# Kernel optimization log

Hardware: AMD Instinct MI355X
Metric: run time of the kernel (lower is better)

## Reference

```python
import jax, jax.numpy as jnp
import numpy as np

TAU = 0.5

def setup_inputs() -> dict:
    key = jax.random.key(0)
    ks = jax.random.split(key, 20)
    B, D1, D2, E1, E2, U = 4096, 2000, 2000, 256, 256, 512
    M = E1 + E2
    s = lambda k, shp, scale=0.05: jax.random.normal(k, shp, dtype=jnp.float32) * scale
    return {
        "inputs": jax.random.normal(ks[0], (B, D1 + D2), dtype=jnp.float32),
        "h_tm1": jax.random.normal(ks[1], (B, U), dtype=jnp.float32),
        "crohis_tm": jax.random.normal(ks[2], (B, M), dtype=jnp.float32),
        "embed_weight_1": s(ks[3], (D1, E1)),
        "embed_weight_2": s(ks[4], (D2, E2)),
        "ca_1to2_w": s(ks[5], (E1, E1)),
        "ca_1to2_u": s(ks[6], (E2, E1)),
        "ca_1to2_v": s(ks[7], (E2, E1)),
        "ca_2to1_w": s(ks[8], (E2, E2)),
        "ca_2to1_u": s(ks[9], (E1, E2)),
        "ca_2to1_v": s(ks[10], (E1, E2)),
        "crohis_weight_w": s(ks[11], (M, U)),
        "crohis_bias": jnp.zeros((U,), jnp.float32),
        "crohis_decomp_weight": s(ks[12], (M, M)),
        "crohis_decomp_bias": jnp.zeros((M,), jnp.float32),
        "kernel": s(ks[13], (M, 3 * U)),
        "recurrent_kernel": s(ks[14], (U, 3 * U)),
        "bias": jnp.zeros((3 * U,), jnp.float32),
    }


def reference(inputs, h_tm1, crohis_tm,
              embed_weight_1, embed_weight_2,
              ca_1to2_w, ca_1to2_u, ca_1to2_v,
              ca_2to1_w, ca_2to1_u, ca_2to1_v,
              crohis_weight_w, crohis_bias,
              crohis_decomp_weight, crohis_decomp_bias,
              kernel, recurrent_kernel, bias):
    D1 = embed_weight_1.shape[0]
    U = recurrent_kernel.shape[0]
    # dual embedding lookups (dense multi-hot x embedding matrix)
    seqx1 = inputs[:, :D1]
    seqx2 = inputs[:, D1:]
    emb1 = seqx1 @ embed_weight_1   # [B, E1]
    emb2 = seqx2 @ embed_weight_2   # [B, E2]
    # cross-attention gates (softmax over feature axis, as K.softmax default)
    att12 = jax.nn.softmax(jnp.tanh(emb1 @ ca_1to2_w + emb2 @ ca_1to2_u) * (emb2 @ ca_1to2_v), axis=-1)
    att21 = jax.nn.softmax(jnp.tanh(emb2 @ ca_2to1_w + emb1 @ ca_2to1_u) * (emb1 @ ca_2to1_v), axis=-1)
    x = jnp.concatenate([emb1 * att12, emb2 * att21], axis=-1)  # [B, M]
    # cross-history decomposition modulating previous hidden state
    cro = jnp.tanh(crohis_tm @ crohis_decomp_weight + crohis_decomp_bias)
    h_prev = h_tm1 + jnp.tanh(cro @ crohis_weight_w + crohis_bias)
    # GRU (implementation=2, reset_after=False)
    mx = x @ kernel + bias                         # [B, 3U]
    x_z, x_r, x_h = mx[:, :U], mx[:, U:2 * U], mx[:, 2 * U:]
    mi = h_prev @ recurrent_kernel[:, :2 * U]      # [B, 2U]
    z = jax.nn.sigmoid(x_z + mi[:, :U])
    r = jax.nn.sigmoid(x_r + mi[:, U:])
    hh = jnp.tanh(x_h + (r * h_prev) @ recurrent_kernel[:, 2 * U:])
    h = z * h_prev + (1.0 - z) * hh
    # updated cross-history state (exponential moving average with tau)
    crohis_new = TAU * crohis_tm + (1.0 - TAU) * x
    return h, crohis_new
```

## Files before the change

kernel.cpp:

```cpp
#include <hip/hip_runtime.h>
#include <hip/hip_bf16.h>
#include <math.h>


#define TAU_F 0.5f

typedef __bf16 bf16x8 __attribute__((ext_vector_type(8)));
typedef __bf16 bf16x4 __attribute__((ext_vector_type(4)));
typedef float f32x4 __attribute__((ext_vector_type(4)));

__device__ __forceinline__ void gload16(const void* g, void* l) {
    __builtin_amdgcn_global_load_lds(
        (const __attribute__((address_space(1))) void*)g,
        (__attribute__((address_space(3))) void*)l, 16, 0, 0);
}

struct SubGemm64 {
    const float* A;
    int lda;
    int Kvalid;
    const __bf16* BT;
    int ldbt;
    float* C;
    int ldc;
    long long strideC;
    int Ksub;
    int nbx;
    int pairSplit;
    int pairAOff;
};

__global__ __launch_bounds__(256) void gemm64_dual(SubGemm64 g1, SubGemm64 g2, int blocks1)
{
    __shared__ __attribute__((aligned(16))) char lds[24576];
    auto As32 = (float (*)[64][32])lds;
    auto Bs   = (__bf16 (*)[64][32])(lds + 16384);

    const int tid = threadIdx.x, w = tid >> 6, l = tid & 63;

    const int gx = gridDim.x;
    const int nwg = gx * (int)gridDim.y;
    const int hw = (int)blockIdx.y * gx + (int)blockIdx.x;
    const int lg = (hw & 7) * (nwg >> 3) + (hw >> 3);
    const int bxl_lin = lg % gx;
    const int by = lg / gx;

    const bool second = bxl_lin >= blocks1;
    const SubGemm64& g = second ? g2 : g1;
    const int bxl = second ? bxl_lin - blocks1 : bxl_lin;
    const int ct = bxl % g.nbx, spl = bxl / g.nbx;
    const int brow = by * 64, bcol = ct * 64;
    const int k_begin = spl * g.Ksub;
    const int nt = g.Ksub >> 5;
    const int aoff = (ct >= g.pairSplit) ? g.pairAOff : 0;

    const float* Ar0 = g.A + aoff + (size_t)(brow + w * 16 + (l >> 3)) * g.lda;
    const float* Ar8 = Ar0 + (size_t)8 * g.lda;
    const int colLane = (l & 7) * 4;
    const int kcl4 = g.Kvalid - 4;
    const __bf16* Bg = g.BT + (size_t)(bcol + w * 16 + (l >> 2)) * g.ldbt
                     + (l & 3) * 8 + k_begin;

    f32x4 acc[2][2] = {};
    const int fr = l & 15, fk = (l >> 4) * 8;
    const int wr = (w >> 1) * 32, wc = (w & 1) * 32;
    const int kmax = (nt - 1) * 32;

#define ISS64(slot)                                                          \
    {                                                                        \
        const int _s = (slot);                                               \
        const int _k = (_s * 32 < kmax) ? _s * 32 : kmax;                    \
        const int _b = _s & 1;                                               \
        int c0 = k_begin + _k + colLane;                                     \
        c0 = c0 < kcl4 ? c0 : kcl4;                                          \
        gload16(Ar0 + c0, &As32[_b][w * 16][0]);                             \
        gload16(Ar8 + c0, &As32[_b][w * 16 + 8][0]);                         \
        gload16(Bg + _k,  &Bs[_b][w * 16][0]);                               \
    }

    ISS64(0) ISS64(1)

    for (int t = 0; t < nt; ++t) {
        asm volatile("s_waitcnt vmcnt(3)" ::: "memory");
        asm volatile("s_waitcnt lgkmcnt(0)" ::: "memory");
        asm volatile("s_barrier" ::: "memory");

        const int bi = t & 1;
        bf16x8 a[2], b[2];
#pragma unroll
        for (int m = 0; m < 2; ++m) {
            f32x4 lo = *(const f32x4*)&As32[bi][wr + m * 16 + fr][fk];
            f32x4 hi = *(const f32x4*)&As32[bi][wr + m * 16 + fr][fk + 4];
#pragma unroll
            for (int z = 0; z < 4; ++z) { a[m][z] = (__bf16)lo[z]; a[m][4 + z] = (__bf16)hi[z]; }
        }
#pragma unroll
        for (int n = 0; n < 2; ++n) b[n] = *(const bf16x8*)&Bs[bi][wc + n * 16 + fr][fk];

#pragma unroll
        for (int m = 0; m < 2; ++m)
#pragma unroll
            for (int n = 0; n < 2; ++n)
                acc[m][n] = __builtin_amdgcn_mfma_f32_16x16x32_bf16(a[m], b[n], acc[m][n], 0, 0, 0);

        asm volatile("s_barrier" ::: "memory");
        ISS64(t + 2)
    }
#undef ISS64

    float* C = g.C + (size_t)spl * g.strideC;
    const int fq = (l >> 4) * 4;
#pragma unroll
    for (int m = 0; m < 2; ++m)
#pragma unroll
        for (int n = 0; n < 2; ++n)
#pragma unroll
            for (int r = 0; r < 4; ++r) {
                int row = brow + wr + m * 16 + fq + r;
                int col = bcol + wc + n * 16 + fr;
                C[(size_t)row * g.ldc + col] = acc[m][n][r];
            }
}

struct SubGemm {
    const void* A;
    int lda;
    int Kvalid;
    const __bf16* BT;
    int ldbt;
    float* C;
    int ldc;
    long long strideC;
    int Ksub;
    int nbx;
    int pairSplit;
    int pairAOff;
    int obf16;
};

__global__ __launch_bounds__(256) void gemm_dual(SubGemm g1, SubGemm g2, int blocks1)
{
    __shared__ __attribute__((aligned(16))) char lds[49152];

    const int tid = threadIdx.x, w = tid >> 6, l = tid & 63;

    const int gx = gridDim.x;
    const int nwg = gx * (int)gridDim.y;
    const int hw = (int)blockIdx.y * gx + (int)blockIdx.x;
    const int lg = (hw & 7) * (nwg >> 3) + (hw >> 3);
    const int bxl_lin = lg % gx;
    const int by = lg / gx;

    const bool second = bxl_lin >= blocks1;
    const SubGemm& g = second ? g2 : g1;
    const int bxl = second ? bxl_lin - blocks1 : bxl_lin;
    const int ct = bxl % g.nbx, spl = bxl / g.nbx;
    const int brow = by * 64, bcol = ct * 128;
    const int k_begin = spl * g.Ksub;
    const int nt = g.Ksub >> 5;
    const int aoff = (ct >= g.pairSplit) ? g.pairAOff : 0;

    const int sbr = w * 32 + (l >> 2);
    const int seg = (l & 3) * 8;

    const __bf16* Bg0 = g.BT + (size_t)(bcol + sbr) * g.ldbt + seg + k_begin;
    const __bf16* Bg1 = Bg0 + (size_t)16 * g.ldbt;

    f32x4 acc[2][4] = {};
    const int fr = l & 15, fk = (l >> 4) * 8;
    const int wr = (w >> 1) * 32, wc = (w & 1) * 64;
    const int kmax = (nt - 1) * 32;

    auto As = (__bf16 (*)[64][32])lds;
    auto Bs = (__bf16 (*)[128][32])(lds + 16384);

    const int sar = w * 16 + (l >> 2);
    const __bf16* Ar = (const __bf16*)g.A + aoff
                     + (size_t)(brow + sar) * g.lda + seg + k_begin;

#define ISSUE_AB(slot)                                                        \
    {                                                                         \
        const int _s = (slot);                                                \
        const int _k = (_s * 32 < kmax) ? _s * 32 : kmax;                     \
        const int _b = _s & 3;                                                \
        gload16(Ar + _k,  &As[_b][w * 16][0]);                                \
        gload16(Bg0 + _k, &Bs[_b][w * 32][0]);                                \
        gload16(Bg1 + _k, &Bs[_b][w * 32 + 16][0]);                           \
    }

    ISSUE_AB(0) ISSUE_AB(1) ISSUE_AB(2)

    for (int t = 0; t < nt; ++t) {
        asm volatile("s_waitcnt vmcnt(6)" ::: "memory");
        asm volatile("s_waitcnt lgkmcnt(0)" ::: "memory");
        __builtin_amdgcn_s_barrier();

        const int bi = t & 3;
        bf16x8 a[2], b[4];
#pragma unroll
        for (int m = 0; m < 2; ++m) a[m] = *(const bf16x8*)&As[bi][wr + m * 16 + fr][fk];
#pragma unroll
        for (int n = 0; n < 4; ++n) b[n] = *(const bf16x8*)&Bs[bi][wc + n * 16 + fr][fk];

        ISSUE_AB(t + 3)

#pragma unroll
        for (int m = 0; m < 2; ++m)
#pragma unroll
            for (int n = 0; n < 4; ++n)
                acc[m][n] = __builtin_amdgcn_mfma_f32_16x16x32_bf16(a[m], b[n], acc[m][n], 0, 0, 0);
    }
#undef ISSUE_AB

    const int fq = (l >> 4) * 4;
    if (g.obf16) {
        __bf16* Cb = (__bf16*)g.C + (size_t)spl * g.strideC;
#pragma unroll
        for (int m = 0; m < 2; ++m)
#pragma unroll
            for (int n = 0; n < 4; ++n)
#pragma unroll
                for (int r = 0; r < 4; ++r) {
                    int row = brow + wr + m * 16 + fq + r;
                    int col = bcol + wc + n * 16 + fr;
                    Cb[(size_t)row * g.ldc + col] = (__bf16)acc[m][n][r];
                }
    } else {
        float* C = g.C + (size_t)spl * g.strideC;
#pragma unroll
        for (int m = 0; m < 2; ++m)
#pragma unroll
            for (int n = 0; n < 4; ++n)
#pragma unroll
                for (int r = 0; r < 4; ++r) {
                    int row = brow + wr + m * 16 + fq + r;
                    int col = bcol + wc + n * 16 + fr;
                    C[(size_t)row * g.ldc + col] = acc[m][n][r];
                }
    }
}

__global__ __launch_bounds__(256) void gemm_g8(
    const __bf16* __restrict__ A, const __bf16* __restrict__ BT,
    const float* __restrict__ mx, const float* __restrict__ mi2,
    const float* __restrict__ hprev, const float* __restrict__ bias,
    float* __restrict__ h)
{
    __shared__ __attribute__((aligned(16))) char lds[49152];

    const int tid = threadIdx.x, w = tid >> 6, l = tid & 63;

    const int gx = gridDim.x;
    const int nwg = gx * (int)gridDim.y;
    const int hw = (int)blockIdx.y * gx + (int)blockIdx.x;
    const int lg = (hw & 7) * (nwg >> 3) + (hw >> 3);
    const int ct = lg % gx;
    const int by = lg / gx;

    const int brow = by * 64, bcol = ct * 128;
    const int nt = 16;

    const int sbr = w * 32 + (l >> 2);
    const int seg = (l & 3) * 8;

    const __bf16* Bg0 = BT + (size_t)(bcol + sbr) * 512 + seg;
    const __bf16* Bg1 = Bg0 + (size_t)16 * 512;

    f32x4 acc[2][4] = {};
    const int fr = l & 15, fk = (l >> 4) * 8;
    const int wr = (w >> 1) * 32, wc = (w & 1) * 64;
    const int kmax = (nt - 1) * 32;

    auto As = (__bf16 (*)[64][32])lds;
    auto Bs = (__bf16 (*)[128][32])(lds + 16384);

    const int sar = w * 16 + (l >> 2);
    const __bf16* Ar = A + (size_t)(brow + sar) * 512 + seg;

#define ISSUE_G8(slot)                                                        \
    {                                                                         \
        const int _s = (slot);                                                \
        const int _k = (_s * 32 < kmax) ? _s * 32 : kmax;                     \
        const int _b = _s & 3;                                                \
        gload16(Ar + _k,  &As[_b][w * 16][0]);                                \
        gload16(Bg0 + _k, &Bs[_b][w * 32][0]);                                \
        gload16(Bg1 + _k, &Bs[_b][w * 32 + 16][0]);                           \
    }

    ISSUE_G8(0) ISSUE_G8(1) ISSUE_G8(2)

    for (int t = 0; t < nt; ++t) {
        asm volatile("s_waitcnt vmcnt(6)" ::: "memory");
        asm volatile("s_waitcnt lgkmcnt(0)" ::: "memory");
        __builtin_amdgcn_s_barrier();

        const int bi = t & 3;
        bf16x8 a[2], b[4];
#pragma unroll
        for (int m = 0; m < 2; ++m) a[m] = *(const bf16x8*)&As[bi][wr + m * 16 + fr][fk];
#pragma unroll
        for (int n = 0; n < 4; ++n) b[n] = *(const bf16x8*)&Bs[bi][wc + n * 16 + fr][fk];

        ISSUE_G8(t + 3)

#pragma unroll
        for (int m = 0; m < 2; ++m)
#pragma unroll
            for (int n = 0; n < 4; ++n)
                acc[m][n] = __builtin_amdgcn_mfma_f32_16x16x32_bf16(a[m], b[n], acc[m][n], 0, 0, 0);
    }
#undef ISSUE_G8

    const int fq = (l >> 4) * 4;
#pragma unroll
    for (int m = 0; m < 2; ++m)
#pragma unroll
        for (int n = 0; n < 4; ++n)
#pragma unroll
            for (int r = 0; r < 4; ++r) {
                int row = brow + wr + m * 16 + fq + r;
                int col = bcol + wc + n * 16 + fr;
                float xz = mx[(size_t)row * 1536 + col]        + bias[col];
                float xh = mx[(size_t)row * 1536 + 1024 + col] + bias[1024 + col];
                float mz = mi2[(size_t)row * 1024 + col];
                float hp = hprev[(size_t)row * 512 + col];
                float z  = 1.f / (1.f + expf(-(xz + mz)));
                float hh = tanhf(xh + acc[m][n][r]);
                h[(size_t)row * 512 + col] = z * hp + (1.f - z) * hh;
            }
}

__global__ __launch_bounds__(256) void prep_wT(
    const float* __restrict__ ew1, const float* __restrict__ ew2,
    const float* __restrict__ w12, const float* __restrict__ u12,
    const float* __restrict__ v12, const float* __restrict__ w21,
    const float* __restrict__ u21, const float* __restrict__ v21,
    const float* __restrict__ cd_w, const float* __restrict__ cw_w,
    const float* __restrict__ kern, const float* __restrict__ rkern,
    __bf16* __restrict__ WT, __bf16* __restrict__ WcatT,
    __bf16* __restrict__ cdT, __bf16* __restrict__ cwT,
    __bf16* __restrict__ kernT, __bf16* __restrict__ rkernT)
{
    __shared__ float tile[64][65];
    const int b = blockIdx.x, tid = threadIdx.x;
    const int tr = tid >> 6, tc = tid & 63;

    const float* src = nullptr;
    int ldsrc = 0, srow0 = 0, scol0 = 0, kvalid = 1 << 30;
    __bf16* dst; int ldd, n0, k0;
    bool zero = false;

    if (b < 256) {
        int q = b; n0 = (q >> 5) * 64; k0 = (q & 31) * 64;
        dst = WT; ldd = 2048; kvalid = 2000; ldsrc = 256; srow0 = k0;
        if (n0 < 256) { src = ew1; scol0 = n0; } else { src = ew2; scol0 = n0 - 256; }
    } else if (b < 384) {
        int q = b - 256; n0 = (q >> 3) * 64; k0 = (q & 7) * 64;
        dst = WcatT; ldd = 512; ldsrc = 256; srow0 = k0 & 255; scol0 = n0 & 255;
        int qn = n0 >> 8; bool khi = k0 >= 256;
        if (qn == 0)      src = khi ? u12 : w12;
        else if (qn == 1) src = khi ? w21 : u21;
        else if (qn == 2) { if (khi) src = v12; else zero = true; }
        else              { if (khi) zero = true; else src = v21; }
    } else if (b < 448) {
        int q = b - 384; n0 = (q >> 3) * 64; k0 = (q & 7) * 64;
        src = cd_w; ldsrc = 512; srow0 = k0; scol0 = n0; dst = cdT; ldd = 512;
    } else if (b < 512) {
        int q = b - 448; n0 = (q >> 3) * 64; k0 = (q & 7) * 64;
        src = cw_w; ldsrc = 512; srow0 = k0; scol0 = n0; dst = cwT; ldd = 512;
    } else if (b < 704) {
        int q = b - 512; n0 = (q >> 3) * 64; k0 = (q & 7) * 64;
        src = kern; ldsrc = 1536; srow0 = k0; scol0 = n0; dst = kernT; ldd = 512;
    } else {
        int q = b - 704; n0 = (q >> 3) * 64; k0 = (q & 7) * 64;
        src = rkern; ldsrc = 1536; srow0 = k0; scol0 = n0; dst = rkernT; ldd = 512;
    }

#pragma unroll
    for (int p = 0; p < 16; ++p) {
        int kr = p * 4 + tr;
        float v = 0.f;
        if (!zero && (srow0 + kr) < kvalid)
            v = src[(size_t)(srow0 + kr) * ldsrc + scol0 + tc];
        tile[kr][tc] = v;
    }
    __syncthreads();
#pragma unroll
    for (int p = 0; p < 16; ++p) {
        int nr = p * 4 + tr;
        dst[(size_t)(n0 + nr) * ldd + k0 + tc] = (__bf16)tile[tc][nr];
    }
}

__global__ __launch_bounds__(256) void reduce_A(
    const float* __restrict__ P12, const float* __restrict__ P4,
    const float* __restrict__ cd_b,
    __bf16* __restrict__ E, __bf16* __restrict__ cro)
{
    const int S = 1 << 21;
    int b = blockIdx.x;
    int i = (((b & 2047) * 256) + threadIdx.x) * 4;
    if (b < 2048) {
        f32x4 p0 = *(const f32x4*)(P12 + i);
        f32x4 p1 = *(const f32x4*)(P12 + S + i);
        f32x4 p2 = *(const f32x4*)(P12 + 2 * S + i);
        f32x4 p3 = *(const f32x4*)(P12 + 3 * S + i);
        __bf16 o[4];
#pragma unroll
        for (int j = 0; j < 4; ++j) o[j] = (__bf16)((p0[j] + p1[j]) + (p2[j] + p3[j]));
        *(bf16x4*)&E[i] = *(bf16x4*)o;
    } else {
        f32x4 p0 = *(const f32x4*)(P4 + i);
        int c = i & 511;
        __bf16 o[4];
#pragma unroll
        for (int j = 0; j < 4; ++j) o[j] = (__bf16)tanhf(p0[j] + cd_b[c + j]);
        *(bf16x4*)&cro[i] = *(bf16x4*)o;
    }
}

__global__ __launch_bounds__(256) void fuse1(
    const __bf16* __restrict__ T, const __bf16* __restrict__ E,
    const float* __restrict__ crohis,
    const float* __restrict__ P5,
    const float* __restrict__ h_tm1, const float* __restrict__ cw_b,
    __bf16* __restrict__ x, float* __restrict__ cro_out,
    float* __restrict__ hprev, __bf16* __restrict__ hprev_bf)
{
    __shared__ float s4[4];
    int b = blockIdx.x;
    int j = threadIdx.x;
    if (b < 4096) {
        const __bf16* t = T + (size_t)b * 1024;
        float s12 = tanhf((float)t[j])       * (float)t[512 + j];
        float s21 = tanhf((float)t[256 + j]) * (float)t[768 + j];
        float v = s12;
#pragma unroll
        for (int o = 32; o >= 1; o >>= 1) v = fmaxf(v, __shfl_xor(v, o, 64));
        __syncthreads(); if ((j & 63) == 0) s4[j >> 6] = v; __syncthreads();
        float m12 = fmaxf(fmaxf(s4[0], s4[1]), fmaxf(s4[2], s4[3]));
        float e12 = expf(s12 - m12);
        v = e12;
#pragma unroll
        for (int o = 32; o >= 1; o >>= 1) v += __shfl_xor(v, o, 64);
        __syncthreads(); if ((j & 63) == 0) s4[j >> 6] = v; __syncthreads();
        float sum12 = s4[0] + s4[1] + s4[2] + s4[3];
        v = s21;
#pragma unroll
        for (int o = 32; o >= 1; o >>= 1) v = fmaxf(v, __shfl_xor(v, o, 64));
        __syncthreads(); if ((j & 63) == 0) s4[j >> 6] = v; __syncthreads();
        float m21 = fmaxf(fmaxf(s4[0], s4[1]), fmaxf(s4[2], s4[3]));
        float e21 = expf(s21 - m21);
        v = e21;
#pragma unroll
        for (int o = 32; o >= 1; o >>= 1) v += __shfl_xor(v, o, 64);
        __syncthreads(); if ((j & 63) == 0) s4[j >> 6] = v; __syncthreads();
        float sum21 = s4[0] + s4[1] + s4[2] + s4[3];

        size_t b0 = (size_t)b * 512 + j, b1 = b0 + 256;
        float x1 = (float)E[b0] * (e12 / sum12);
        float x2 = (float)E[b1] * (e21 / sum21);
        x[b0] = (__bf16)x1;
        x[b1] = (__bf16)x2;
        cro_out[b0] = TAU_F * crohis[b0] + (1.f - TAU_F) * x1;
        cro_out[b1] = TAU_F * crohis[b1] + (1.f - TAU_F) * x2;
    } else {
        int i = ((b - 4096) * 256 + j) * 4;
        f32x4 p = *(const f32x4*)(P5 + i);
        f32x4 ht = *(const f32x4*)(h_tm1 + i);
        int c = i & 511;
        f32x4 o; __bf16 ob[4];
#pragma unroll
        for (int q = 0; q < 4; ++q) {
            float hv = ht[q] + tanhf(p[q] + cw_b[c + q]);
            o[q] = hv; ob[q] = (__bf16)hv;
        }
        *(f32x4*)(hprev + i) = o;
        *(bf16x4*)&hprev_bf[i] = *(bf16x4*)ob;
    }
}

__global__ __launch_bounds__(256) void gates_k(
    const float* __restrict__ mx, const float* __restrict__ mi2,
    const float* __restrict__ hprev, const float* __restrict__ bias,
    __bf16* __restrict__ rh)
{
    int i = (blockIdx.x * 256 + threadIdx.x) * 4;
    int row = i >> 9, c = i & 511;
    f32x4 a  = *(const f32x4*)(mx + (size_t)row * 1536 + 512 + c);
    f32x4 m  = *(const f32x4*)(mi2 + (size_t)row * 1024 + 512 + c);
    f32x4 hp = *(const f32x4*)(hprev + i);
    f32x4 bb = *(const f32x4*)(bias + 512 + c);
    __bf16 o[4];
#pragma unroll
    for (int q = 0; q < 4; ++q) {
        float r = 1.f / (1.f + expf(-(a[q] + bb[q] + m[q])));
        o[q] = (__bf16)(r * hp[q]);
    }
    *(bf16x4*)&rh[i] = *(bf16x4*)o;
}

extern "C" void kernel_launch(void* const* d_in, const int* in_sizes, int n_in,
                              void* d_out, int out_size, void* d_ws, size_t ws_size,
                              hipStream_t stream)
{
    (void)in_sizes; (void)n_in; (void)out_size; (void)ws_size;

    const float* inputs = (const float*)d_in[0];
    const float* h_tm1  = (const float*)d_in[1];
    const float* crohis = (const float*)d_in[2];
    const float* ew1    = (const float*)d_in[3];
    const float* ew2    = (const float*)d_in[4];
    const float* ca12w  = (const float*)d_in[5];
    const float* ca12u  = (const float*)d_in[6];
    const float* ca12v  = (const float*)d_in[7];
    const float* ca21w  = (const float*)d_in[8];
    const float* ca21u  = (const float*)d_in[9];
    const float* ca21v  = (const float*)d_in[10];
    const float* cw_w   = (const float*)d_in[11];
    const float* cw_b   = (const float*)d_in[12];
    const float* cd_w   = (const float*)d_in[13];
    const float* cd_b   = (const float*)d_in[14];
    const float* kern   = (const float*)d_in[15];
    const float* rkern  = (const float*)d_in[16];
    const float* bias   = (const float*)d_in[17];

    char* ws = (char*)d_ws;
    const size_t MB = 1 << 20;
    float*  P12      = (float*)(ws + 0);
    float*  mx       = (float*)(ws + 0);
    float*  P4       = (float*)(ws + 32 * MB);
    __bf16* T        = (__bf16*)(ws + 32 * MB);
    float*  mi2      = (float*)(ws + 24 * MB);
    float*  P5       = (float*)(ws + 40 * MB);
    __bf16* x        = (__bf16*)(ws + 48 * MB);
    __bf16* rh       = (__bf16*)(ws + 48 * MB);
    __bf16* E        = (__bf16*)(ws + 52 * MB);
    __bf16* cro_bf   = (__bf16*)(ws + 56 * MB);
    float*  hprev    = (float*)(ws + 60 * MB);
    __bf16* hprev_bf = (__bf16*)(ws + 68 * MB);
    __bf16* WT       = (__bf16*)(ws + 72 * MB);
    __bf16* WcatT    = (__bf16*)(ws + 74 * MB);
    __bf16* cdT      = (__bf16*)(ws + 75 * MB);
    __bf16* cwT      = (__bf16*)(ws + 75 * MB + 512 * 1024);
    __bf16* kernT    = (__bf16*)(ws + 76 * MB);
    __bf16* rkernT   = (__bf16*)(ws + 77 * MB + 512 * 1024);

    float* h_out   = (float*)d_out;
    float* cro_out = (float*)d_out + 2 * 1048576;

    const int BIG = 1 << 30;
    const long long S2 = 1ll << 21;

    prep_wT<<<896, 256, 0, stream>>>(ew1, ew2, ca12w, ca12u, ca12v, ca21w,
                                     ca21u, ca21v, cd_w, cw_w, kern, rkern,
                                     WT, WcatT, cdT, cwT, kernT, rkernT);

    SubGemm64 gA1 = { inputs, 4000, 2000, WT,  2048, P12, 512, S2, 512, 8, 4,   2000 };
    SubGemm64 gA2 = { crohis,  512,  512, cdT,  512, P4,  512, 0,  512, 8, BIG, 0 };
    gemm64_dual<<<dim3(40, 64), 256, 0, stream>>>(gA1, gA2, 32);

    reduce_A<<<4096, 256, 0, stream>>>(P12, P4, cd_b, E, cro_bf);

    SubGemm gB1 = { E,      512, 512, WcatT, 512, (float*)T, 1024, 0, 512, 8, BIG, 0, 1 };
    SubGemm gB2 = { cro_bf, 512, 512, cwT,   512, P5,        512,  0, 512, 4, BIG, 0, 0 };
    gemm_dual<<<dim3(12, 64), 256, 0, stream>>>(gB1, gB2, 8);

    fuse1<<<6144, 256, 0, stream>>>(T, E, crohis, P5, h_tm1, cw_b,
                                    x, cro_out, hprev, hprev_bf);

    SubGemm gC1 = { x,        512, 512, kernT,  512, mx,  1536, 0, 512, 12, BIG, 0, 0 };
    SubGemm gC2 = { hprev_bf, 512, 512, rkernT, 512, mi2, 1024, 0, 512, 8,  BIG, 0, 0 };
    gemm_dual<<<dim3(20, 64), 256, 0, stream>>>(gC1, gC2, 12);

    gates_k<<<2048, 256, 0, stream>>>(mx, mi2, hprev, bias, rh);

    gemm_g8<<<dim3(4, 64), 256, 0, stream>>>(
        rh, rkernT + (size_t)1024 * 512, mx, mi2, hprev, bias, h_out);
}
```

Before: 143.7 us.

## Enlarge first-stage GEMM tiles to 64x128x64 and halve the split-K partials

The embedding/crohis GEMM kernel moves from 64x64 tiles with K-step 32 to 64x128 tiles with K-step 64. Each stage now issues more loads and twice the MFMAs per wave. Split-K for the embedding GEMM drops from 4 to 2, so the reduce kernel reads two partial buffers instead of four, and the workspace layout is compacted to match. The aim is more data reuse per block and less partial-sum traffic. The cost is 64KB of LDS per block and a grid of 768 blocks instead of 2560, which lowers occupancy and parallelism.

```diff
diff --git a/kernel.cpp b/kernel.cpp
--- a/kernel.cpp
+++ b/kernel.cpp
@@ -15,7 +15,7 @@
         (__attribute__((address_space(3))) void*)l, 16, 0, 0);
 }
 
-struct SubGemm64 {
+struct SubGemmA {
     const float* A;
     int lda;
     int Kvalid;
@@ -30,11 +30,11 @@
     int pairAOff;
 };
 
-__global__ __launch_bounds__(256) void gemm64_dual(SubGemm64 g1, SubGemm64 g2, int blocks1)
-{
-    __shared__ __attribute__((aligned(16))) char lds[24576];
-    auto As32 = (float (*)[64][32])lds;
-    auto Bs   = (__bf16 (*)[64][32])(lds + 16384);
+__global__ __launch_bounds__(256) void gemmA_dual(SubGemmA g1, SubGemmA g2, int blocks1)
+{
+    __shared__ __attribute__((aligned(16))) char lds[65536];
+    auto Af = (float (*)[64][64])lds;
+    auto Bs = (__bf16 (*)[128][64])(lds + 32768);
 
     const int tid = threadIdx.x, w = tid >> 6, l = tid & 63;
 
@@ -46,74 +46,90 @@
     const int by = lg / gx;
 
     const bool second = bxl_lin >= blocks1;
-    const SubGemm64& g = second ? g2 : g1;
+    const SubGemmA& g = second ? g2 : g1;
     const int bxl = second ? bxl_lin - blocks1 : bxl_lin;
     const int ct = bxl % g.nbx, spl = bxl / g.nbx;
-    const int brow = by * 64, bcol = ct * 64;
+    const int brow = by * 64, bcol = ct * 128;
     const int k_begin = spl * g.Ksub;
-    const int nt = g.Ksub >> 5;
+    const int nt = g.Ksub >> 6;
     const int aoff = (ct >= g.pairSplit) ? g.pairAOff : 0;
 
-    const float* Ar0 = g.A + aoff + (size_t)(brow + w * 16 + (l >> 3)) * g.lda;
-    const float* Ar8 = Ar0 + (size_t)8 * g.lda;
-    const int colLane = (l & 7) * 4;
-    const int kcl4 = g.Kvalid - 4;
-    const __bf16* Bg = g.BT + (size_t)(bcol + w * 16 + (l >> 2)) * g.ldbt
-                     + (l & 3) * 8 + k_begin;
-
-    f32x4 acc[2][2] = {};
+    const float* ArA = g.A + aoff + (size_t)(brow + w * 16 + (l >> 4)) * g.lda;
+    const int acol = (l & 15) * 4;
+    const int kclA = g.Kvalid - 4;
+    const __bf16* BrB = g.BT + (size_t)(bcol + w * 32 + (l >> 3)) * g.ldbt
+                      + (l & 7) * 8 + k_begin;
+
+    f32x4 acc[2][4] = {};
     const int fr = l & 15, fk = (l >> 4) * 8;
-    const int wr = (w >> 1) * 32, wc = (w & 1) * 32;
-    const int kmax = (nt - 1) * 32;
-
-#define ISS64(slot)                                                          \
+    const int wr = (w >> 1) * 32, wc = (w & 1) * 64;
+    const int kmaxk = (nt - 1) * 64;
+
+#define ISSA(slot)                                                           \
     {                                                                        \
         const int _s = (slot);                                               \
-        const int _k = (_s * 32 < kmax) ? _s * 32 : kmax;                    \
+        const int _k = (_s * 64 < kmaxk) ? _s * 64 : kmaxk;                  \
         const int _b = _s & 1;                                               \
-        int c0 = k_begin + _k + colLane;                                     \
-        c0 = c0 < kcl4 ? c0 : kcl4;                                          \
-        gload16(Ar0 + c0, &As32[_b][w * 16][0]);                             \
-        gload16(Ar8 + c0, &As32[_b][w * 16 + 8][0]);                         \
-        gload16(Bg + _k,  &Bs[_b][w * 16][0]);                               \
-    }
-
-    ISS64(0) ISS64(1)
+        int c0 = k_begin + _k + acol;                                        \
+        c0 = c0 < kclA ? c0 : kclA;                                          \
+        gload16(ArA + c0,               &Af[_b][w * 16][0]);                 \
+        gload16(ArA + 4 * g.lda + c0,   &Af[_b][w * 16 + 4][0]);             \
+        gload16(ArA + 8 * g.lda + c0,   &Af[_b][w * 16 + 8][0]);             \
+        gload16(ArA + 12 * g.lda + c0,  &Af[_b][w * 16 + 12][0]);            \
+        gload16(BrB + _k,               &Bs[_b][w * 32][0]);                 \
+        gload16(BrB + 8 * g.ldbt + _k,  &Bs[_b][w * 32 + 8][0]);             \
+        gload16(BrB + 16 * g.ldbt + _k, &Bs[_b][w * 32 + 16][0]);            \
+        gload16(BrB + 24 * g.ldbt + _k, &Bs[_b][w * 32 + 24][0]);            \
+    }
+
+    ISSA(0) ISSA(1)
 
     for (int t = 0; t < nt; ++t) {
-        asm volatile("s_waitcnt vmcnt(3)" ::: "memory");
+        asm volatile("s_waitcnt vmcnt(8)" ::: "memory");
         asm volatile("s_waitcnt lgkmcnt(0)" ::: "memory");
-        asm volatile("s_barrier" ::: "memory");
+        __builtin_amdgcn_s_barrier();
 
         const int bi = t & 1;
-        bf16x8 a[2], b[2];
+        bf16x8 a0[2], a1[2], b0[4], b1[4];
 #pragma unroll
         for (int m = 0; m < 2; ++m) {
-            f32x4 lo = *(const f32x4*)&As32[bi][wr + m * 16 + fr][fk];
-            f32x4 hi = *(const f32x4*)&As32[bi][wr + m * 16 + fr][fk + 4];
-#pragma unroll
-            for (int z = 0; z < 4; ++z) { a[m][z] = (__bf16)lo[z]; a[m][4 + z] = (__bf16)hi[z]; }
+            const float* rp = &Af[bi][wr + m * 16 + fr][0];
+            f32x4 lo = *(const f32x4*)(rp + fk);
+            f32x4 hi = *(const f32x4*)(rp + fk + 4);
+            f32x4 lo2 = *(const f32x4*)(rp + 32 + fk);
+            f32x4 hi2 = *(const f32x4*)(rp + 32 + fk + 4);
+#pragma unroll
+            for (int z = 0; z < 4; ++z) {
+                a0[m][z] = (__bf16)lo[z];  a0[m][4 + z] = (__bf16)hi[z];
+                a1[m][z] = (__bf16)lo2[z]; a1[m][4 + z] = (__bf16)hi2[z];
+            }
         }
 #pragma unroll
-        for (int n = 0; n < 2; ++n) b[n] = *(const bf16x8*)&Bs[bi][wc + n * 16 + fr][fk];
+        for (int n = 0; n < 4; ++n) {
+            const __bf16* rp = &Bs[bi][wc + n * 16 + fr][0];
+            b0[n] = *(const bf16x8*)(rp + fk);
+            b1[n] = *(const bf16x8*)(rp + 32 + fk);
+        }
 
 #pragma unroll
         for (int m = 0; m < 2; ++m)
 #pragma unroll
-            for (int n = 0; n < 2; ++n)
-                acc[m][n] = __builtin_amdgcn_mfma_f32_16x16x32_bf16(a[m], b[n], acc[m][n], 0, 0, 0);
-
-        asm volatile("s_barrier" ::: "memory");
-        ISS64(t + 2)
-    }
-#undef ISS64
+            for (int n = 0; n < 4; ++n) {
+                acc[m][n] = __builtin_amdgcn_mfma_f32_16x16x32_bf16(a0[m], b0[n], acc[m][n], 0, 0, 0);
+                acc[m][n] = __builtin_amdgcn_mfma_f32_16x16x32_bf16(a1[m], b1[n], acc[m][n], 0, 0, 0);
+            }
+
+        __builtin_amdgcn_s_barrier();
+        ISSA(t + 2)
+    }
+#undef ISSA
 
     float* C = g.C + (size_t)spl * g.strideC;
     const int fq = (l >> 4) * 4;
 #pragma unroll
     for (int m = 0; m < 2; ++m)
 #pragma unroll
-        for (int n = 0; n < 2; ++n)
+        for (int n = 0; n < 4; ++n)
 #pragma unroll
             for (int r = 0; r < 4; ++r) {
                 int row = brow + wr + m * 16 + fq + r;
@@ -403,11 +419,9 @@
     if (b < 2048) {
         f32x4 p0 = *(const f32x4*)(P12 + i);
         f32x4 p1 = *(const f32x4*)(P12 + S + i);
-        f32x4 p2 = *(const f32x4*)(P12 + 2 * S + i);
-        f32x4 p3 = *(const f32x4*)(P12 + 3 * S + i);
         __bf16 o[4];
 #pragma unroll
-        for (int j = 0; j < 4; ++j) o[j] = (__bf16)((p0[j] + p1[j]) + (p2[j] + p3[j]));
+        for (int j = 0; j < 4; ++j) o[j] = (__bf16)(p0[j] + p1[j]);
         *(bf16x4*)&E[i] = *(bf16x4*)o;
     } else {
         f32x4 p0 = *(const f32x4*)(P4 + i);
@@ -528,17 +542,17 @@
     char* ws = (char*)d_ws;
     const size_t MB = 1 << 20;
     float*  P12      = (float*)(ws + 0);
-    float*  mx       = (float*)(ws + 0);
-    float*  P4       = (float*)(ws + 32 * MB);
-    __bf16* T        = (__bf16*)(ws + 32 * MB);
-    float*  mi2      = (float*)(ws + 24 * MB);
-    float*  P5       = (float*)(ws + 40 * MB);
-    __bf16* x        = (__bf16*)(ws + 48 * MB);
-    __bf16* rh       = (__bf16*)(ws + 48 * MB);
-    __bf16* E        = (__bf16*)(ws + 52 * MB);
-    __bf16* cro_bf   = (__bf16*)(ws + 56 * MB);
+    float*  P4       = (float*)(ws + 16 * MB);
+    __bf16* T        = (__bf16*)(ws + 16 * MB);
+    float*  P5       = (float*)(ws + 32 * MB);
+    __bf16* x        = (__bf16*)(ws + 40 * MB);
+    __bf16* rh       = (__bf16*)(ws + 40 * MB);
+    __bf16* E        = (__bf16*)(ws + 48 * MB);
+    __bf16* cro_bf   = (__bf16*)(ws + 52 * MB);
     float*  hprev    = (float*)(ws + 60 * MB);
     __bf16* hprev_bf = (__bf16*)(ws + 68 * MB);
+    float*  mx       = (float*)(ws + 0);
+    float*  mi2      = (float*)(ws + 24 * MB);
     __bf16* WT       = (__bf16*)(ws + 72 * MB);
     __bf16* WcatT    = (__bf16*)(ws + 74 * MB);
     __bf16* cdT      = (__bf16*)(ws + 75 * MB);
@@ -556,9 +570,9 @@
                                      ca21u, ca21v, cd_w, cw_w, kern, rkern,
                                      WT, WcatT, cdT, cwT, kernT, rkernT);
 
-    SubGemm64 gA1 = { inputs, 4000, 2000, WT,  2048, P12, 512, S2, 512, 8, 4,   2000 };
-    SubGemm64 gA2 = { crohis,  512,  512, cdT,  512, P4,  512, 0,  512, 8, BIG, 0 };
-    gemm64_dual<<<dim3(40, 64), 256, 0, stream>>>(gA1, gA2, 32);
+    SubGemmA gA1 = { inputs, 4000, 2000, WT,  2048, P12, 512, S2, 1024, 4, 2,   2000 };
+    SubGemmA gA2 = { crohis,  512,  512, cdT,  512, P4,  512, 0,   512, 4, BIG, 0 };
+    gemmA_dual<<<dim3(12, 64), 256, 0, stream>>>(gA1, gA2, 8);
 
     reduce_A<<<4096, 256, 0, stream>>>(P12, P4, cd_b, E, cro_bf);
 
```

Measured after the change: 150.6 us, median of 2. 1.05x slower.
